# Optimization experiments

Hardware: AMD Instinct MI355X
Metric: run time of the kernel (lower is better)

## Reference

```python
import jax, jax.numpy as jnp
import numpy as np

N, E, H, C = 50000, 800000, 4, 32   # nodes, edges, heads, per-head channels
HID, LAT, G = H * C, 32, 128        # hidden, latent, num graphs
IN_DIM = 64
NEG_SLOPE = 0.2
BN_EPS = 1e-5


def setup_inputs() -> dict:
    key = jax.random.key(0)
    ks = jax.random.split(key, 20)
    inp = {
        "x": jax.random.normal(ks[0], (N, IN_DIM), jnp.float32),
        "edge_index": jax.random.randint(ks[1], (2, E), 0, N, jnp.int32),
        "batch": jnp.sort(jax.random.randint(ks[2], (N,), 0, G, jnp.int32)),
        # layer 0
        "W0": jax.random.normal(ks[3], (IN_DIM, HID), jnp.float32) * (1.0 / np.sqrt(IN_DIM)),
        "a_src0": jax.random.normal(ks[4], (H, C), jnp.float32) * 0.1,
        "a_dst0": jax.random.normal(ks[5], (H, C), jnp.float32) * 0.1,
        "b0": jnp.zeros((HID,), jnp.float32),
        # layer 1
        "W1": jax.random.normal(ks[6], (HID, HID), jnp.float32) * (1.0 / np.sqrt(HID)),
        "a_src1": jax.random.normal(ks[7], (H, C), jnp.float32) * 0.1,
        "a_dst1": jax.random.normal(ks[8], (H, C), jnp.float32) * 0.1,
        "b1": jnp.zeros((HID,), jnp.float32),
        # layer 2
        "W2": jax.random.normal(ks[9], (HID, HID), jnp.float32) * (1.0 / np.sqrt(HID)),
        "a_src2": jax.random.normal(ks[10], (H, C), jnp.float32) * 0.1,
        "a_dst2": jax.random.normal(ks[11], (H, C), jnp.float32) * 0.1,
        "b2": jnp.zeros((HID,), jnp.float32),
        # head
        "fc_w": jax.random.normal(ks[12], (HID, LAT), jnp.float32) * (1.0 / np.sqrt(HID)),
        "fc_b": jnp.zeros((LAT,), jnp.float32),
        "bn_g": jnp.ones((LAT,), jnp.float32),
        "bn_b": jnp.zeros((LAT,), jnp.float32),
    }
    return inp


def _gat_conv(x, src, dst, W, a_src, a_dst, b):
    n = x.shape[0]
    h = (x @ W).reshape(n, H, C)                      # [N,H,C]
    alpha_s = jnp.einsum("nhc,hc->nh", h, a_src)       # [N,H]
    alpha_d = jnp.einsum("nhc,hc->nh", h, a_dst)
    e = jax.nn.leaky_relu(alpha_s[src] + alpha_d[dst], NEG_SLOPE)  # [E',H]
    # scatter-softmax over incoming edges of each dst node
    m = jax.ops.segment_max(e, dst, num_segments=n)
    m = jnp.where(jnp.isfinite(m), m, 0.0)
    ex = jnp.exp(e - m[dst])
    denom = jax.ops.segment_sum(ex, dst, num_segments=n)
    alpha = ex / (denom[dst] + 1e-16)                  # [E',H]
    out = jax.ops.segment_sum(alpha[:, :, None] * h[src], dst, num_segments=n)
    return out.reshape(n, H * C) + b


def reference(x, edge_index, batch, W0, a_src0, a_dst0, b0, W1, a_src1, a_dst1, b1,
              W2, a_src2, a_dst2, b2, fc_w, fc_b, bn_g, bn_b):
    # PyG GATConv default add_self_loops=True
    loop = jnp.arange(N, dtype=edge_index.dtype)
    src = jnp.concatenate([edge_index[0], loop])
    dst = jnp.concatenate([edge_index[1], loop])

    h = x
    for (W, a_s, a_d, b) in ((W0, a_src0, a_dst0, b0),
                             (W1, a_src1, a_dst1, b1),
                             (W2, a_src2, a_dst2, b2)):
        h = _gat_conv(h, src, dst, W, a_s, a_d, b)
        h = jax.nn.leaky_relu(h, NEG_SLOPE)  # dropout is identity in eval

    pooled = jax.ops.segment_sum(h, batch, num_segments=G)  # global_add_pool -> [G,HID]
    out = pooled @ fc_w + fc_b
    # BatchNorm1d in eval mode with running_mean=0, running_var=1
    out = bn_g * out * (1.0 / np.sqrt(1.0 + BN_EPS)) + bn_b
    return out
```

## Files before the change

### kernel.cpp

```cpp
#include <hip/hip_runtime.h>
#include <hip/hip_bf16.h>
#include <float.h>

#define NEG 0.2f
#define SEGSHIFT 13

__device__ __forceinline__ float leaky(float x) { return x > 0.0f ? x : NEG * x; }

__device__ __forceinline__ unsigned short f2bf(float f) {
  unsigned x = __float_as_uint(f);
  unsigned r = (x + 0x7fffu + ((x >> 16) & 1u)) >> 16;
  return (unsigned short)r;
}

__device__ __forceinline__ float2 bf2f2(unsigned u) {
  float2 r;
  r.x = __uint_as_float(u << 16);
  r.y = __uint_as_float(u & 0xffff0000u);
  return r;
}

using frag8 = __attribute__((ext_vector_type(8))) short;
using f32x4v = __attribute__((ext_vector_type(4))) float;

__global__ void zero_kernel(int* __restrict__ p, int n) {
  int i = blockIdx.x * blockDim.x + threadIdx.x;
  int stride = gridDim.x * blockDim.x;
  for (; i < n; i += stride) p[i] = 0;
}

__global__ void xcvt_kernel(const float* __restrict__ x, unsigned short* __restrict__ xb, int n) {
  int i = blockIdx.x * blockDim.x + threadIdx.x;
  if (i < n) xb[i] = f2bf(x[i]);
}

__global__ void count_kernel(const int* __restrict__ ei, int* __restrict__ degseg,
                             int E, int N, int nseg) {
  int i = blockIdx.x * blockDim.x + threadIdx.x;
  if (i >= E + N) return;
  int src, dst;
  if (i < E) { src = ei[i]; dst = ei[E + i]; } else { src = dst = i - E; }
  atomicAdd(&degseg[(size_t)dst * nseg + (src >> SEGSHIFT)], 1);
}

__global__ __launch_bounds__(1024) void scan_block_kernel(const int* __restrict__ deg,
                                                          int* __restrict__ row_start,
                                                          int* __restrict__ sums, int n) {
  __shared__ int buf[1024];
  int t = threadIdx.x;
  int idx = blockIdx.x * 1024 + t;
  int x = (idx < n) ? deg[idx] : 0;
  int v = x;
  buf[t] = v;
  __syncthreads();
  for (int off = 1; off < 1024; off <<= 1) {
    int a = (t >= off) ? buf[t - off] : 0;
    __syncthreads();
    v += a;
    buf[t] = v;
    __syncthreads();
  }
  if (idx < n) row_start[idx] = v - x;
  if (t == 1023) sums[blockIdx.x] = v;
}

__global__ __launch_bounds__(1024) void scan_sums_kernel(int* __restrict__ sums,
                                                         int* __restrict__ row_start,
                                                         int nch, int n) {
  __shared__ int buf[1024];
  int t = threadIdx.x;
  int x = (t < nch) ? sums[t] : 0;
  int v = x;
  buf[t] = v;
  __syncthreads();
  for (int off = 1; off < 1024; off <<= 1) {
    int a = (t >= off) ? buf[t - off] : 0;
    __syncthreads();
    v += a;
    buf[t] = v;
    __syncthreads();
  }
  if (t < nch) sums[t] = v - x;
  if (t == 1023) row_start[n] = v;
}

__global__ __launch_bounds__(1024) void scan_add_kernel(int* __restrict__ row_start,
                                                        const int* __restrict__ sums, int n) {
  int idx = blockIdx.x * 1024 + threadIdx.x;
  if (idx < n) row_start[idx] += sums[blockIdx.x];
}

__global__ void fill_kernel(const int* __restrict__ ei, int* __restrict__ cursor,
                            const int* __restrict__ rowseg, int* __restrict__ csr_src,
                            int* __restrict__ csr_dst, int E, int N, int nseg) {
  int i = blockIdx.x * blockDim.x + threadIdx.x;
  if (i >= E + N) return;
  int src, dst;
  if (i < E) { src = ei[i]; dst = ei[E + i]; } else { src = dst = i - E; }
  size_t b = (size_t)dst * nseg + (src >> SEGSHIFT);
  int pos = atomicAdd(&cursor[b], 1);
  int slot = rowseg[b] + pos;
  csr_src[slot] = src;
  csr_dst[slot] = dst;
}

__global__ __launch_bounds__(256) void gemm_kernel(const unsigned short* __restrict__ Xb,
                                                   const float* __restrict__ W,
                                                   unsigned short* __restrict__ Hb,
                                                   const float* __restrict__ a_src,
                                                   const float* __restrict__ a_dst,
                                                   float* __restrict__ as_arr,
                                                   float* __restrict__ ad_arr,
                                                   int nrows, int K) {
  __shared__ unsigned short Wt[128][136];
  __shared__ unsigned short Xs[64][136];
  int t = threadIdx.x;
  int wave = t >> 6, lane = t & 63;
  int n0 = lane & 15, quad = lane >> 4;
  int row0 = blockIdx.x * 64, wrow = wave * 16;

  for (int idx = t; idx < K * 128; idx += 256) {
    int k = idx >> 7, n = idx & 127;
    Wt[n][k] = f2bf(W[idx]);
  }
  int rowElems = K >> 3;
  for (int idx = t; idx < 64 * rowElems; idx += 256) {
    int r = idx / rowElems, c8 = idx % rowElems;
    int gr = row0 + r;
    uint4 v = make_uint4(0, 0, 0, 0);
    if (gr < nrows) v = *(const uint4*)(Xb + (size_t)gr * K + c8 * 8);
    *(uint4*)(&Xs[r][c8 * 8]) = v;
  }
  __syncthreads();

  f32x4v acc[8];
#pragma unroll
  for (int c = 0; c < 8; ++c) acc[c] = (f32x4v){0.f, 0.f, 0.f, 0.f};

  for (int kb = 0; kb < K; kb += 32) {
    frag8 a = *(const frag8*)(&Xs[wrow + n0][kb + quad * 8]);
#pragma unroll
    for (int c = 0; c < 8; ++c) {
      frag8 b = *(const frag8*)(&Wt[c * 16 + n0][kb + quad * 8]);
      acc[c] = __builtin_amdgcn_mfma_f32_16x16x32_bf16(a, b, acc[c], 0, 0, 0);
    }
  }

  float asv[8], adv[8];
#pragma unroll
  for (int c = 0; c < 8; ++c) {
    asv[c] = a_src[c * 16 + n0];
    adv[c] = a_dst[c * 16 + n0];
  }
#pragma unroll
  for (int r = 0; r < 4; ++r) {
    float ps[4] = {0.f, 0.f, 0.f, 0.f}, pd[4] = {0.f, 0.f, 0.f, 0.f};
#pragma unroll
    for (int c = 0; c < 8; ++c) {
      int h = c >> 1;
      ps[h] += acc[c][r] * asv[c];
      pd[h] += acc[c][r] * adv[c];
    }
#pragma unroll
    for (int off = 1; off < 16; off <<= 1) {
#pragma unroll
      for (int h = 0; h < 4; ++h) {
        ps[h] += __shfl_xor(ps[h], off);
        pd[h] += __shfl_xor(pd[h], off);
      }
    }
    if (n0 == 0) {
      int m = row0 + wrow + quad * 4 + r;
      if (m < nrows) {
#pragma unroll
        for (int h = 0; h < 4; ++h) {
          as_arr[(size_t)m * 4 + h] = ps[h];
          ad_arr[(size_t)m * 4 + h] = pd[h];
        }
      }
    }
  }

  __syncthreads();
#pragma unroll
  for (int c = 0; c < 8; ++c)
#pragma unroll
    for (int r = 0; r < 4; ++r)
      Xs[wrow + quad * 4 + r][c * 16 + n0] = f2bf(acc[c][r]);
  __syncthreads();
  for (int idx = t; idx < 64 * 16; idx += 256) {
    int r = idx >> 4, c8 = idx & 15;
    int gr = row0 + r;
    if (gr < nrows)
      *(uint4*)(Hb + (size_t)gr * 128 + c8 * 8) = *(const uint4*)(&Xs[r][c8 * 8]);
  }
}

__global__ __launch_bounds__(256) void ecomp_kernel(const int* __restrict__ csr_src,
                                                    const int* __restrict__ csr_dst,
                                                    const float* __restrict__ as_arr,
                                                    const float* __restrict__ ad_arr,
                                                    float* __restrict__ earr, int Etot) {
  int i = blockIdx.x * 256 + threadIdx.x;
  if (i >= Etot) return;
  int s = csr_src[i];
  int d = csr_dst[i];
  float4 a = *(const float4*)(as_arr + (size_t)s * 4);
  float4 b = *(const float4*)(ad_arr + (size_t)d * 4);
  float4 e;
  e.x = __expf(fminf(leaky(a.x + b.x), 80.f));
  e.y = __expf(fminf(leaky(a.y + b.y), 80.f));
  e.z = __expf(fminf(leaky(a.z + b.z), 80.f));
  e.w = __expf(fminf(leaky(a.w + b.w), 80.f));
  *(float4*)(earr + (size_t)i * 4) = e;
}

template <int POOL>
__global__ __launch_bounds__(256) void agg_kernel(const unsigned short* __restrict__ Hb,
                                                  const float* __restrict__ earr,
                                                  const int* __restrict__ csr_src,
                                                  const int* __restrict__ rowseg,
                                                  const float* __restrict__ bias,
                                                  unsigned short* __restrict__ xnext,
                                                  const int* __restrict__ batch,
                                                  float* __restrict__ pooled,
                                                  int N, int nseg) {
  int wid = threadIdx.x >> 6;
  int lane = threadIdx.x & 63;
  int n = blockIdx.x * 4 + wid;
  if (n >= N) return;
  int rs = rowseg[(size_t)n * nseg];
  int re = rowseg[(size_t)n * nseg + nseg];
  int head = lane >> 4;

  const unsigned* hp = (const unsigned*)Hb + lane;
  const float* ep = earr + head;
  float denom = 0.f, acc0 = 0.f, acc1 = 0.f;
  int i = rs;
  for (; i + 4 <= re; i += 4) {
    int s0 = csr_src[i], s1 = csr_src[i + 1], s2 = csr_src[i + 2], s3 = csr_src[i + 3];
    float e0 = ep[(size_t)i * 4];
    float e1 = ep[(size_t)(i + 1) * 4];
    float e2 = ep[(size_t)(i + 2) * 4];
    float e3 = ep[(size_t)(i + 3) * 4];
    unsigned u0 = hp[(size_t)s0 * 64];
    unsigned u1 = hp[(size_t)s1 * 64];
    unsigned u2 = hp[(size_t)s2 * 64];
    unsigned u3 = hp[(size_t)s3 * 64];
    denom += (e0 + e1) + (e2 + e3);
    float2 f;
    f = bf2f2(u0); acc0 += e0 * f.x; acc1 += e0 * f.y;
    f = bf2f2(u1); acc0 += e1 * f.x; acc1 += e1 * f.y;
    f = bf2f2(u2); acc0 += e2 * f.x; acc1 += e2 * f.y;
    f = bf2f2(u3); acc0 += e3 * f.x; acc1 += e3 * f.y;
  }
  for (; i < re; ++i) {
    int s0 = csr_src[i];
    float e0 = ep[(size_t)i * 4];
    unsigned u0 = hp[(size_t)s0 * 64];
    float2 f = bf2f2(u0);
    denom += e0;
    acc0 += e0 * f.x;
    acc1 += e0 * f.y;
  }
  float inv = 1.0f / (denom + 1e-16f);
  float2 bv = *(const float2*)(bias + 2 * lane);
  float v0 = leaky(acc0 * inv + bv.x);
  float v1 = leaky(acc1 * inv + bv.y);
  if (POOL) {
    int g = batch[n];
    atomicAdd(&pooled[(size_t)g * 128 + 2 * lane], v0);
    atomicAdd(&pooled[(size_t)g * 128 + 2 * lane + 1], v1);
  } else {
    unsigned pk = ((unsigned)f2bf(v1) << 16) | (unsigned)f2bf(v0);
    ((unsigned*)xnext)[(size_t)n * 64 + lane] = pk;
  }
}

__global__ void head_kernel(const float* __restrict__ pooled, const float* __restrict__ fc_w,
                            const float* __restrict__ fc_b, const float* __restrict__ bn_g,
                            const float* __restrict__ bn_b, float* __restrict__ out, int G) {
  int t = threadIdx.x;
  int g = blockIdx.x * 8 + (t >> 5);
  int j = t & 31;
  if (g >= G) return;
  const float* pr = pooled + (size_t)g * 128;
  float acc = 0.f;
#pragma unroll 8
  for (int k = 0; k < 128; ++k) acc += pr[k] * fc_w[k * 32 + j];
  const float inv = 0.9999950000374997f;
  out[g * 32 + j] = bn_g[j] * (acc + fc_b[j]) * inv + bn_b[j];
}

extern "C" void kernel_launch(void* const* d_in, const int* in_sizes, int n_in,
                              void* d_out, int out_size, void* d_ws, size_t ws_size,
                              hipStream_t stream) {
  const float* x = (const float*)d_in[0];
  const int* ei = (const int*)d_in[1];
  const int* batch = (const int*)d_in[2];
  const float* Wm[3] = {(const float*)d_in[3], (const float*)d_in[7], (const float*)d_in[11]};
  const float* a_s[3] = {(const float*)d_in[4], (const float*)d_in[8], (const float*)d_in[12]};
  const float* a_d[3] = {(const float*)d_in[5], (const float*)d_in[9], (const float*)d_in[13]};
  const float* bb[3] = {(const float*)d_in[6], (const float*)d_in[10], (const float*)d_in[14]};
  const float* fc_w = (const float*)d_in[15];
  const float* fc_b = (const float*)d_in[16];
  const float* bn_g = (const float*)d_in[17];
  const float* bn_b = (const float*)d_in[18];
  float* out = (float*)d_out;

  int N = in_sizes[0] / 64;
  int E = in_sizes[1] / 2;
  int G = out_size / 32;
  int Etot = E + N;
  int nseg = ((N - 1) >> SEGSHIFT) + 1;
  int L = N * nseg;

  char* p = (char*)d_ws;
  auto carve = [&](size_t bytes) {
    char* r = p;
    p += (bytes + 255) & ~size_t(255);
    return r;
  };
  int* degseg    = (int*)carve((size_t)L * 4);
  int* cursor    = (int*)carve((size_t)L * 4);
  float* pooled  = (float*)carve((size_t)G * 128 * 4);
  int* rowseg    = (int*)carve((size_t)(L + 1) * 4);
  int* sums      = (int*)carve(4096);
  int* csr_src   = (int*)carve((size_t)Etot * 4);
  int* csr_dst   = (int*)carve((size_t)Etot * 4);
  float* earr    = (float*)carve((size_t)Etot * 4 * 4);
  unsigned short* Hb = (unsigned short*)carve((size_t)N * 128 * 2);
  unsigned short* Xb = (unsigned short*)carve((size_t)N * 128 * 2);
  float* as_arr  = (float*)carve((size_t)N * 4 * 4);
  float* ad_arr  = (float*)carve((size_t)N * 4 * 4);

  int nz = (int)(((char*)(pooled + (size_t)G * 128) - (char*)degseg) / 4);
  zero_kernel<<<512, 256, 0, stream>>>(degseg, nz);

  xcvt_kernel<<<(N * 64 + 255) / 256, 256, 0, stream>>>(x, Xb, N * 64);

  int egrid = (Etot + 255) / 256;
  count_kernel<<<egrid, 256, 0, stream>>>(ei, degseg, E, N, nseg);
  int nch = (L + 1023) / 1024;
  scan_block_kernel<<<nch, 1024, 0, stream>>>(degseg, rowseg, sums, L);
  scan_sums_kernel<<<1, 1024, 0, stream>>>(sums, rowseg, nch, L);
  scan_add_kernel<<<nch, 1024, 0, stream>>>(rowseg, sums, L);
  fill_kernel<<<egrid, 256, 0, stream>>>(ei, cursor, rowseg, csr_src, csr_dst, E, N, nseg);

  int ggrid = (N + 63) / 64;
  int ngrid = (N + 3) / 4;

  gemm_kernel<<<ggrid, 256, 0, stream>>>(Xb, Wm[0], Hb, a_s[0], a_d[0], as_arr, ad_arr, N, 64);
  ecomp_kernel<<<egrid, 256, 0, stream>>>(csr_src, csr_dst, as_arr, ad_arr, earr, Etot);
  agg_kernel<0><<<ngrid, 256, 0, stream>>>(Hb, earr, csr_src, rowseg, bb[0],
                                           Xb, nullptr, nullptr, N, nseg);
  gemm_kernel<<<ggrid, 256, 0, stream>>>(Xb, Wm[1], Hb, a_s[1], a_d[1], as_arr, ad_arr, N, 128);
  ecomp_kernel<<<egrid, 256, 0, stream>>>(csr_src, csr_dst, as_arr, ad_arr, earr, Etot);
  agg_kernel<0><<<ngrid, 256, 0, stream>>>(Hb, earr, csr_src, rowseg, bb[1],
                                           Xb, nullptr, nullptr, N, nseg);
  gemm_kernel<<<ggrid, 256, 0, stream>>>(Xb, Wm[2], Hb, a_s[2], a_d[2], as_arr, ad_arr, N, 128);
  ecomp_kernel<<<egrid, 256, 0, stream>>>(csr_src, csr_dst, as_arr, ad_arr, earr, Etot);
  agg_kernel<1><<<ngrid, 256, 0, stream>>>(Hb, earr, csr_src, rowseg, bb[2],
                                           nullptr, batch, pooled, N, nseg);

  head_kernel<<<(G + 7) / 8, 256, 0, stream>>>(pooled, fc_w, fc_b, bn_g, bn_b, out, G);
}
```

Before: 472.8 us.

## Split H and edge weights into per-head planes, aggregate one head per block

The GEMM now writes H in a head-major layout ([4][N][32] bf16), and ecomp writes edge weights as four per-head planes. The aggregation grid becomes 4x larger with one head per block, and each wave handles one node-head pair. The four 16-lane quarters of a wave process different edges in parallel and are combined with shuffles. The aim is better L2 locality for each head's H slice and more edge-level parallelism for low-degree nodes. The cost is four reads of the CSR index arrays instead of one, uncoalesced scalar edge-weight stores, and an extra reduction step.

New measurement: 579.5 us. 1.23x slower.

```diff
diff --git a/kernel.cpp b/kernel.cpp
--- a/kernel.cpp
+++ b/kernel.cpp
@@ -106,7 +106,7 @@
 
 __global__ __launch_bounds__(256) void gemm_kernel(const unsigned short* __restrict__ Xb,
                                                    const float* __restrict__ W,
-                                                   unsigned short* __restrict__ Hb,
+                                                   unsigned short* __restrict__ Hh,
                                                    const float* __restrict__ a_src,
                                                    const float* __restrict__ a_dst,
                                                    float* __restrict__ as_arr,
@@ -192,7 +192,8 @@
     int r = idx >> 4, c8 = idx & 15;
     int gr = row0 + r;
     if (gr < nrows)
-      *(uint4*)(Hb + (size_t)gr * 128 + c8 * 8) = *(const uint4*)(&Xs[r][c8 * 8]);
+      *(uint4*)(Hh + ((size_t)(c8 >> 2) * nrows + gr) * 32 + (c8 & 3) * 8) =
+          *(const uint4*)(&Xs[r][c8 * 8]);
   }
 }
 
@@ -200,80 +201,74 @@
                                                     const int* __restrict__ csr_dst,
                                                     const float* __restrict__ as_arr,
                                                     const float* __restrict__ ad_arr,
-                                                    float* __restrict__ earr, int Etot) {
+                                                    float* __restrict__ eh, int Etot) {
   int i = blockIdx.x * 256 + threadIdx.x;
   if (i >= Etot) return;
   int s = csr_src[i];
   int d = csr_dst[i];
   float4 a = *(const float4*)(as_arr + (size_t)s * 4);
   float4 b = *(const float4*)(ad_arr + (size_t)d * 4);
-  float4 e;
-  e.x = __expf(fminf(leaky(a.x + b.x), 80.f));
-  e.y = __expf(fminf(leaky(a.y + b.y), 80.f));
-  e.z = __expf(fminf(leaky(a.z + b.z), 80.f));
-  e.w = __expf(fminf(leaky(a.w + b.w), 80.f));
-  *(float4*)(earr + (size_t)i * 4) = e;
+  eh[i]                    = __expf(fminf(leaky(a.x + b.x), 80.f));
+  eh[(size_t)Etot + i]     = __expf(fminf(leaky(a.y + b.y), 80.f));
+  eh[(size_t)2 * Etot + i] = __expf(fminf(leaky(a.z + b.z), 80.f));
+  eh[(size_t)3 * Etot + i] = __expf(fminf(leaky(a.w + b.w), 80.f));
 }
 
 template <int POOL>
-__global__ __launch_bounds__(256) void agg_kernel(const unsigned short* __restrict__ Hb,
-                                                  const float* __restrict__ earr,
+__global__ __launch_bounds__(256) void agg_kernel(const unsigned short* __restrict__ Hh,
+                                                  const float* __restrict__ eh,
                                                   const int* __restrict__ csr_src,
                                                   const int* __restrict__ rowseg,
                                                   const float* __restrict__ bias,
                                                   unsigned short* __restrict__ xnext,
                                                   const int* __restrict__ batch,
                                                   float* __restrict__ pooled,
-                                                  int N, int nseg) {
+                                                  int N, int nseg, int Etot, int nb) {
   int wid = threadIdx.x >> 6;
   int lane = threadIdx.x & 63;
-  int n = blockIdx.x * 4 + wid;
+  int q = lane >> 4, ql = lane & 15;
+  int h = blockIdx.x / nb;
+  int n = (blockIdx.x % nb) * 4 + wid;
   if (n >= N) return;
   int rs = rowseg[(size_t)n * nseg];
   int re = rowseg[(size_t)n * nseg + nseg];
-  int head = lane >> 4;
-
-  const unsigned* hp = (const unsigned*)Hb + lane;
-  const float* ep = earr + head;
-  float denom = 0.f, acc0 = 0.f, acc1 = 0.f;
-  int i = rs;
-  for (; i + 4 <= re; i += 4) {
-    int s0 = csr_src[i], s1 = csr_src[i + 1], s2 = csr_src[i + 2], s3 = csr_src[i + 3];
-    float e0 = ep[(size_t)i * 4];
-    float e1 = ep[(size_t)(i + 1) * 4];
-    float e2 = ep[(size_t)(i + 2) * 4];
-    float e3 = ep[(size_t)(i + 3) * 4];
-    unsigned u0 = hp[(size_t)s0 * 64];
-    unsigned u1 = hp[(size_t)s1 * 64];
-    unsigned u2 = hp[(size_t)s2 * 64];
-    unsigned u3 = hp[(size_t)s3 * 64];
-    denom += (e0 + e1) + (e2 + e3);
-    float2 f;
-    f = bf2f2(u0); acc0 += e0 * f.x; acc1 += e0 * f.y;
-    f = bf2f2(u1); acc0 += e1 * f.x; acc1 += e1 * f.y;
-    f = bf2f2(u2); acc0 += e2 * f.x; acc1 += e2 * f.y;
-    f = bf2f2(u3); acc0 += e3 * f.x; acc1 += e3 * f.y;
-  }
-  for (; i < re; ++i) {
-    int s0 = csr_src[i];
-    float e0 = ep[(size_t)i * 4];
-    unsigned u0 = hp[(size_t)s0 * 64];
-    float2 f = bf2f2(u0);
-    denom += e0;
-    acc0 += e0 * f.x;
-    acc1 += e0 * f.y;
-  }
-  float inv = 1.0f / (denom + 1e-16f);
-  float2 bv = *(const float2*)(bias + 2 * lane);
-  float v0 = leaky(acc0 * inv + bv.x);
-  float v1 = leaky(acc1 * inv + bv.y);
-  if (POOL) {
-    int g = batch[n];
-    atomicAdd(&pooled[(size_t)g * 128 + 2 * lane], v0);
-    atomicAdd(&pooled[(size_t)g * 128 + 2 * lane + 1], v1);
-  } else {
-    unsigned pk = ((unsigned)f2bf(v1) << 16) | (unsigned)f2bf(v0);
-    ((unsigned*)xnext)[(size_t)n * 64 + lane] = pk;
+
+  const unsigned* hb = (const unsigned*)Hh + (size_t)h * N * 16;
+  const float* ep = eh + (size_t)h * Etot;
+  float acc0 = 0.f, acc1 = 0.f, den = 0.f;
+
+  for (int i = rs; i < re; i += 8) {
+    int i0 = i + q, i1 = i + 4 + q;
+    int j0 = i0 < re ? i0 : rs;
+    int j1 = i1 < re ? i1 : rs;
+    int s0 = csr_src[j0], s1 = csr_src[j1];
+    float e0 = i0 < re ? ep[j0] : 0.f;
+    float e1 = i1 < re ? ep[j1] : 0.f;
+    unsigned u0 = hb[(size_t)s0 * 16 + ql];
+    unsigned u1 = hb[(size_t)s1 * 16 + ql];
+    float2 f0 = bf2f2(u0), f1 = bf2f2(u1);
+    den += e0 + e1;
+    acc0 += e0 * f0.x + e1 * f1.x;
+    acc1 += e0 * f0.y + e1 * f1.y;
+  }
+  acc0 += __shfl_xor(acc0, 16); acc0 += __shfl_xor(acc0, 32);
+  acc1 += __shfl_xor(acc1, 16); acc1 += __shfl_xor(acc1, 32);
+  den  += __shfl_xor(den, 16);  den  += __shfl_xor(den, 32);
+
+  if (q == 0) {
+    float inv = 1.0f / (den + 1e-16f);
+    int ch = h * 32 + 2 * ql;
+    float2 bv = *(const float2*)(bias + ch);
+    float v0 = leaky(acc0 * inv + bv.x);
+    float v1 = leaky(acc1 * inv + bv.y);
+    if (POOL) {
+      int g = batch[n];
+      atomicAdd(&pooled[(size_t)g * 128 + ch], v0);
+      atomicAdd(&pooled[(size_t)g * 128 + ch + 1], v1);
+    } else {
+      unsigned pk = ((unsigned)f2bf(v1) << 16) | (unsigned)f2bf(v0);
+      ((unsigned*)xnext)[(size_t)n * 64 + h * 16 + ql] = pk;
+    }
   }
 }
 
@@ -328,8 +323,8 @@
   int* sums      = (int*)carve(4096);
   int* csr_src   = (int*)carve((size_t)Etot * 4);
   int* csr_dst   = (int*)carve((size_t)Etot * 4);
-  float* earr    = (float*)carve((size_t)Etot * 4 * 4);
-  unsigned short* Hb = (unsigned short*)carve((size_t)N * 128 * 2);
+  float* eh      = (float*)carve((size_t)Etot * 4 * 4);
+  unsigned short* Hh = (unsigned short*)carve((size_t)N * 128 * 2);
   unsigned short* Xb = (unsigned short*)carve((size_t)N * 128 * 2);
   float* as_arr  = (float*)carve((size_t)N * 4 * 4);
   float* ad_arr  = (float*)carve((size_t)N * 4 * 4);
@@ -348,20 +343,21 @@
   fill_kernel<<<egrid, 256, 0, stream>>>(ei, cursor, rowseg, csr_src, csr_dst, E, N, nseg);
 
   int ggrid = (N + 63) / 64;
-  int ngrid = (N + 3) / 4;
-
-  gemm_kernel<<<ggrid, 256, 0, stream>>>(Xb, Wm[0], Hb, a_s[0], a_d[0], as_arr, ad_arr, N, 64);
-  ecomp_kernel<<<egrid, 256, 0, stream>>>(csr_src, csr_dst, as_arr, ad_arr, earr, Etot);
-  agg_kernel<0><<<ngrid, 256, 0, stream>>>(Hb, earr, csr_src, rowseg, bb[0],
-                                           Xb, nullptr, nullptr, N, nseg);
-  gemm_kernel<<<ggrid, 256, 0, stream>>>(Xb, Wm[1], Hb, a_s[1], a_d[1], as_arr, ad_arr, N, 128);
-  ecomp_kernel<<<egrid, 256, 0, stream>>>(csr_src, csr_dst, as_arr, ad_arr, earr, Etot);
-  agg_kernel<0><<<ngrid, 256, 0, stream>>>(Hb, earr, csr_src, rowseg, bb[1],
-                                           Xb, nullptr, nullptr, N, nseg);
-  gemm_kernel<<<ggrid, 256, 0, stream>>>(Xb, Wm[2], Hb, a_s[2], a_d[2], as_arr, ad_arr, N, 128);
-  ecomp_kernel<<<egrid, 256, 0, stream>>>(csr_src, csr_dst, as_arr, ad_arr, earr, Etot);
-  agg_kernel<1><<<ngrid, 256, 0, stream>>>(Hb, earr, csr_src, rowseg, bb[2],
-                                           nullptr, batch, pooled, N, nseg);
+  int nb = (N + 3) / 4;
+  int ngrid = 4 * nb;
+
+  gemm_kernel<<<ggrid, 256, 0, stream>>>(Xb, Wm[0], Hh, a_s[0], a_d[0], as_arr, ad_arr, N, 64);
+  ecomp_kernel<<<egrid, 256, 0, stream>>>(csr_src, csr_dst, as_arr, ad_arr, eh, Etot);
+  agg_kernel<0><<<ngrid, 256, 0, stream>>>(Hh, eh, csr_src, rowseg, bb[0],
+                                           Xb, nullptr, nullptr, N, nseg, Etot, nb);
+  gemm_kernel<<<ggrid, 256, 0, stream>>>(Xb, Wm[1], Hh, a_s[1], a_d[1], as_arr, ad_arr, N, 128);
+  ecomp_kernel<<<egrid, 256, 0, stream>>>(csr_src, csr_dst, as_arr, ad_arr, eh, Etot);
+  agg_kernel<0><<<ngrid, 256, 0, stream>>>(Hh, eh, csr_src, rowseg, bb[1],
+                                           Xb, nullptr, nullptr, N, nseg, Etot, nb);
+  gemm_kernel<<<ggrid, 256, 0, stream>>>(Xb, Wm[2], Hh, a_s[2], a_d[2], as_arr, ad_arr, N, 128);
+  ecomp_kernel<<<egrid, 256, 0, stream>>>(csr_src, csr_dst, as_arr, ad_arr, eh, Etot);
+  agg_kernel<1><<<ngrid, 256, 0, stream>>>(Hh, eh, csr_src, rowseg, bb[2],
+                                           nullptr, batch, pooled, N, nseg, Etot, nb);
 
   head_kernel<<<(G + 7) / 8, 256, 0, stream>>>(pooled, fc_w, fc_b, bn_g, bn_b, out, G);
 }
```
